# Kernel optimization log

Measured on AMD Instinct MI355X. Metric: run time of the kernel, lower is better.

The kernel has to match this reference:

```python
import jax, jax.numpy as jnp
import numpy as np

H = 56; W = 56; WS = 7; SHIFT = 3; HEADS = 4; C = 128; B = 64
N = WS * WS            # 49 tokens per window
NW = (H // WS) * (W // WS)  # 64 windows per image
HD = C // HEADS
EPS = 1e-5


def _rel_index():
    # matches get_relative_index: pairwise coord diffs in [-(WS-1), WS-1];
    # torch negative indexing wraps, so take mod (2*WS-1)
    coords = np.array([[i, j] for i in range(WS) for j in range(WS)])
    rel = coords[None, :, :] - coords[:, None, :]          # (N, N, 2)
    return (rel % (2 * WS - 1)).astype(np.int32)


def _attn_mask():
    # matches get_attn_mask for shifted windows
    img = np.zeros((H, W))
    sl = (slice(0, -WS), slice(-WS, -SHIFT), slice(-SHIFT, None))
    cnt = 0
    for hs in sl:
        for ws_ in sl:
            img[hs, ws_] = cnt
            cnt += 1
    m = img.reshape(H // WS, WS, W // WS, WS).transpose(0, 2, 1, 3).reshape(NW, N)
    am = m[:, None, :] - m[:, :, None]                     # (NW, N, N)
    return np.where(am != 0, -100.0, 0.0).astype(np.float32)

_REL_IDX = _rel_index()
_MASK = _attn_mask()


def _layernorm(x, g, b):
    mu = jnp.mean(x, axis=-1, keepdims=True)
    var = jnp.mean(jnp.square(x - mu), axis=-1, keepdims=True)
    return (x - mu) * jax.lax.rsqrt(var + EPS) * g + b


def setup_inputs() -> dict:
    key = jax.random.key(0)
    ks = jax.random.split(key, 16)
    s = 0.02
    return {
        "x": jax.random.normal(ks[0], (B, H * W, C), jnp.float32),
        "wq": jax.random.normal(ks[1], (C, C), jnp.float32) * s,
        "bq": jnp.zeros((C,), jnp.float32),
        "wk": jax.random.normal(ks[2], (C, C), jnp.float32) * s,
        "bk": jnp.zeros((C,), jnp.float32),
        "wv": jax.random.normal(ks[3], (C, C), jnp.float32) * s,
        "bv": jnp.zeros((C,), jnp.float32),
        "wo": jax.random.normal(ks[4], (C, C), jnp.float32) * s,
        "bo": jnp.zeros((C,), jnp.float32),
        "rel_table": jax.random.normal(ks[5], (2 * WS - 1, 2 * WS - 1, HEADS), jnp.float32) * s,
        "ln1_g": jnp.ones((C,), jnp.float32),
        "ln1_b": jnp.zeros((C,), jnp.float32),
        "ln2_g": jnp.ones((C,), jnp.float32),
        "ln2_b": jnp.zeros((C,), jnp.float32),
        "w1": jax.random.normal(ks[6], (C, 4 * C), jnp.float32) * s,
        "b1": jnp.zeros((4 * C,), jnp.float32),
        "w2": jax.random.normal(ks[7], (4 * C, C), jnp.float32) * s,
        "b2": jnp.zeros((C,), jnp.float32),
    }


def reference(x, wq, bq, wk, bk, wv, bv, wo, bo, rel_table,
              ln1_g, ln1_b, ln2_g, ln2_b, w1, b1, w2, b2):
    shortcut = x                                     # (B, H*W, C)
    h = _layernorm(x, ln1_g, ln1_b).reshape(B, H, W, C)
    h = jnp.roll(h, (-SHIFT, -SHIFT), axis=(1, 2))   # cyclic shift
    # window partition -> (B*NW, N, C)
    h = h.reshape(B, H // WS, WS, W // WS, WS, C).transpose(0, 1, 3, 2, 4, 5)
    h = h.reshape(B * NW, N, C)
    q = (h @ wq + bq).reshape(B * NW, N, HEADS, HD)
    k = (h @ wk + bk).reshape(B * NW, N, HEADS, HD)
    v = (h @ wv + bv).reshape(B * NW, N, HEADS, HD)
    attn = jnp.einsum('nqhd,nkhd->nhqk', q, k) / np.sqrt(HD).astype(np.float32)
    bias = rel_table[_REL_IDX[:, :, 0], _REL_IDX[:, :, 1]]  # (N, N, HEADS)
    attn = attn + jnp.transpose(bias, (2, 0, 1))[None]      # (1, H, N, N)
    # shifted-window additive mask
    attn = attn.reshape(B, NW, HEADS, N, N) + jnp.asarray(_MASK)[None, :, None]
    attn = jax.nn.softmax(attn.reshape(B * NW, HEADS, N, N), axis=-1)
    out = jnp.einsum('nhqk,nkhd->nqhd', attn, v).reshape(B * NW, N, C)
    out = out @ wo + bo
    # faithful to source bug: output taken directly from window-ordered tokens
    h = out.reshape(B, H * W, C)
    h = h + shortcut
    m = _layernorm(h, ln2_g, ln2_b)
    m = jax.nn.gelu(m @ w1 + b1, approximate=False) @ w2 + b2
    return h + m
```

## Files before the change

kernel.cpp:

```cpp
#include <hip/hip_runtime.h>

typedef __attribute__((ext_vector_type(8))) short short8;
typedef __attribute__((ext_vector_type(4))) float f32x4;
typedef unsigned short u16;
typedef unsigned int u32;

#define MFMA16(a, b, c) __builtin_amdgcn_mfma_f32_16x16x32_bf16((a), (b), (c), 0, 0, 0)
#define SCALE_Q 0.1767766952966369f

__device__ __forceinline__ u16 f2bf(float x) {
  u32 u = __float_as_uint(x);
  u32 r = u + 0x7FFF + ((u >> 16) & 1);
  return (u16)(r >> 16);
}

__device__ __forceinline__ void stage128(u16* lds, const u16* __restrict__ g, int stride, int tid) {
#pragma unroll
  for (int it = 0; it < 8; ++it) {
    int i = it * 256 + tid;
    int row = i >> 4, slot = i & 15;
    short8 v = *(const short8*)(g + row * stride + slot * 8);
    int byte_ = ((row << 8) + (slot << 4)) ^ ((row & 7) << 4);
    *(short8*)((char*)lds + byte_) = v;
  }
}

__device__ __forceinline__ short8 fld256(const u16* lds, int row, int kb) {
  int byte_ = ((row << 8) + kb) ^ ((row & 7) << 4);
  return *(const short8*)((const char*)lds + byte_);
}

__device__ __forceinline__ float gelu_f(float x) {
  float u = 0.7978845608f * (x + 0.044715f * x * x * x);
  float e = __expf(2.f * u);
  float t = 1.f - 2.f / (e + 1.f);
  return 0.5f * x * (1.f + t);
}

__global__ __launch_bounds__(256) void k0_weights(
    const float* __restrict__ wq, const float* __restrict__ wk, const float* __restrict__ wv,
    const float* __restrict__ wo, const float* __restrict__ w1, const float* __restrict__ w2,
    const float* __restrict__ bq, const float* __restrict__ bk, const float* __restrict__ bv,
    u16* __restrict__ wqkvt, u16* __restrict__ wot, u16* __restrict__ w1t, u16* __restrict__ w2t,
    float* __restrict__ bqkv) {
  int idx = blockIdx.x * 256 + threadIdx.x;
  if (idx < 49152) {
    int n = idx >> 7, k = idx & 127;
    float v;
    if (n < 128) v = wq[k * 128 + n] * SCALE_Q;
    else if (n < 256) v = wk[k * 128 + (n - 128)];
    else v = wv[k * 128 + (n - 256)];
    wqkvt[idx] = f2bf(v);
  } else if (idx < 65536) {
    int j = idx - 49152;
    int n = j >> 7, k = j & 127;
    wot[j] = f2bf(wo[k * 128 + n]);
  } else if (idx < 131072) {
    int j = idx - 65536;
    int n = j >> 7, k = j & 127;
    w1t[j] = f2bf(w1[k * 512 + n]);
  } else if (idx < 196608) {
    int j = idx - 131072;
    int n = j >> 9, k = j & 511;
    w2t[j] = f2bf(w2[k * 128 + n]);
  } else if (idx < 196992) {
    int n = idx - 196608;
    float v;
    if (n < 128) v = bq[n] * SCALE_Q;
    else if (n < 256) v = bk[n - 128];
    else v = bv[n - 256];
    bqkv[n] = v;
  }
}

__global__ __launch_bounds__(256) void k0_biasmask(const float* __restrict__ rel, float* __restrict__ bm) {
  int idx = blockIdx.x * 256 + threadIdx.x;
  int reg = idx & 3;
  int lane = (idx >> 2) & 63;
  int nt = (idx >> 8) & 3;
  int mt = (idx >> 10) & 3;
  int h = (idx >> 12) & 3;
  int wi = idx >> 14;
  int r = mt * 16 + ((lane >> 4) << 2) + reg;
  int c = nt * 16 + (lane & 15);
  float v = -1e30f;
  if (r < 49 && c < 49) {
    int qr = r / 7, qc = r % 7, kr = c / 7, kc = c % 7;
    int i0 = (kr - qr + 13) % 13, i1 = (kc - qc + 13) % 13;
    v = rel[(i0 * 13 + i1) * 4 + h];
    int gh = (wi >> 3) * 7 + qr, gw = (wi & 7) * 7 + qc;
    int kh = (wi >> 3) * 7 + kr, kw = (wi & 7) * 7 + kc;
    int rq = (gh < 49 ? 0 : (gh < 53 ? 1 : 2)) * 3 + (gw < 49 ? 0 : (gw < 53 ? 1 : 2));
    int rk = (kh < 49 ? 0 : (kh < 53 ? 1 : 2)) * 3 + (kw < 49 ? 0 : (kw < 53 ? 1 : 2));
    if (rq != rk) v -= 100.f;
  }
  bm[idx] = v;
}

__global__ __launch_bounds__(256) void k1_ln1(const float* __restrict__ x, const float* __restrict__ g,
                                              const float* __restrict__ b, u16* __restrict__ hwin) {
  int wid = threadIdx.x >> 6, lane = threadIdx.x & 63;
  int t = blockIdx.x * 4 + wid;
  float2 v = *(const float2*)(x + t * 128 + lane * 2);
  float s = v.x + v.y;
#pragma unroll
  for (int o = 1; o < 64; o <<= 1) s += __shfl_xor(s, o);
  float mu = s * 0.0078125f;
  float dx = v.x - mu, dy = v.y - mu;
  float q = dx * dx + dy * dy;
#pragma unroll
  for (int o = 1; o < 64; o <<= 1) q += __shfl_xor(q, o);
  float rstd = rsqrtf(q * 0.0078125f + 1e-5f);
  float y0 = dx * rstd * g[lane * 2] + b[lane * 2];
  float y1 = dy * rstd * g[lane * 2 + 1] + b[lane * 2 + 1];
  int bi = t / 3136, hw = t - bi * 3136;
  int oh = hw / 56, ow = hw - oh * 56;
  int gh = oh - 3; if (gh < 0) gh += 56;
  int gw = ow - 3; if (gw < 0) gw += 56;
  int win = bi * 64 + (gh / 7) * 8 + gw / 7;
  int n = (gh % 7) * 7 + (gw % 7);
  u32 packed = (u32)f2bf(y0) | ((u32)f2bf(y1) << 16);
  *(u32*)(hwin + (win * 49 + n) * 128 + lane * 2) = packed;
}

__global__ __launch_bounds__(256) void k2_qkv(const u16* __restrict__ hwin, const u16* __restrict__ wt,
                                              const float* __restrict__ bqkv, u16* __restrict__ qb,
                                              u16* __restrict__ kb, u16* __restrict__ vt) {
  __shared__ u16 lA[128 * 128];
  __shared__ u16 lB[128 * 128];
  int tid = threadIdx.x, mb = blockIdx.x, nb = blockIdx.y;
  stage128(lA, hwin + mb * 128 * 128, 128, tid);
  stage128(lB, wt + nb * 128 * 128, 128, tid);
  __syncthreads();
  int lane = tid & 63, w = tid >> 6;
  int wr = (w >> 1) * 64, wc = (w & 1) * 64;
  int g = lane >> 4, l15 = lane & 15;
  const f32x4 vz = {0.f, 0.f, 0.f, 0.f};
  f32x4 acc[4][4];
#pragma unroll
  for (int i = 0; i < 4; ++i)
#pragma unroll
    for (int j = 0; j < 4; ++j) acc[i][j] = vz;
#pragma unroll
  for (int kt = 0; kt < 4; ++kt) {
    short8 a[4], bfr[4];
#pragma unroll
    for (int mt = 0; mt < 4; ++mt) a[mt] = fld256(lA, wr + mt * 16 + l15, kt * 64 + g * 16);
#pragma unroll
    for (int nt = 0; nt < 4; ++nt) bfr[nt] = fld256(lB, wc + nt * 16 + l15, kt * 64 + g * 16);
#pragma unroll
    for (int mt = 0; mt < 4; ++mt)
#pragma unroll
      for (int nt = 0; nt < 4; ++nt) acc[mt][nt] = MFMA16(a[mt], bfr[nt], acc[mt][nt]);
  }
#pragma unroll
  for (int mt = 0; mt < 4; ++mt)
#pragma unroll
    for (int nt = 0; nt < 4; ++nt) {
      int ng = nb * 128 + wc + nt * 16 + l15;
      float bias = bqkv[ng];
#pragma unroll
      for (int reg = 0; reg < 4; ++reg) {
        int token = mb * 128 + wr + mt * 16 + g * 4 + reg;
        u16 hv = f2bf(acc[mt][nt][reg] + bias);
        if (nb == 0) qb[token * 128 + ng] = hv;
        else if (nb == 1) kb[token * 128 + ng - 128] = hv;
        else {
          int c = ng - 256;
          int win = token / 49, nn = token - win * 49;
          vt[win * 8192 + c * 64 + nn] = hv;
        }
      }
    }
}

__global__ __launch_bounds__(256) void k3_attn(const u16* __restrict__ qb, const u16* __restrict__ kb,
                                               const u16* __restrict__ vt, const float* __restrict__ bm,
                                               u16* __restrict__ ao) {
  __shared__ u16 pl[4 * 4096];
  int win = blockIdx.x;
  int lane = threadIdx.x & 63, head = threadIdx.x >> 6;
  int g = lane >> 4, l15 = lane & 15;
  u16* myp = pl + head * 4096;
  short8 aq[4], bk_[4];
#pragma unroll
  for (int mt = 0; mt < 4; ++mt)
    aq[mt] = *(const short8*)(qb + (win * 49 + mt * 16 + l15) * 128 + head * 32 + g * 8);
#pragma unroll
  for (int nt = 0; nt < 4; ++nt)
    bk_[nt] = *(const short8*)(kb + (win * 49 + nt * 16 + l15) * 128 + head * 32 + g * 8);
  const f32x4* bmv = (const f32x4*)bm + ((win & 63) * 4 + head) * 1024;
  f32x4 s[4][4];
#pragma unroll
  for (int mt = 0; mt < 4; ++mt)
#pragma unroll
    for (int nt = 0; nt < 4; ++nt) s[mt][nt] = bmv[(mt * 4 + nt) * 64 + lane];
#pragma unroll
  for (int mt = 0; mt < 4; ++mt)
#pragma unroll
    for (int nt = 0; nt < 4; ++nt) s[mt][nt] = MFMA16(aq[mt], bk_[nt], s[mt][nt]);
#pragma unroll
  for (int mt = 0; mt < 4; ++mt)
#pragma unroll
    for (int reg = 0; reg < 4; ++reg) {
      float m = fmaxf(fmaxf(s[mt][0][reg], s[mt][1][reg]), fmaxf(s[mt][2][reg], s[mt][3][reg]));
#pragma unroll
      for (int o = 1; o < 16; o <<= 1) m = fmaxf(m, __shfl_xor(m, o));
      float p0 = __expf(s[mt][0][reg] - m);
      float p1 = __expf(s[mt][1][reg] - m);
      float p2 = __expf(s[mt][2][reg] - m);
      float p3 = __expf(s[mt][3][reg] - m);
      float sum = p0 + p1 + p2 + p3;
#pragma unroll
      for (int o = 1; o < 16; o <<= 1) sum += __shfl_xor(sum, o);
      float rinv = 1.f / sum;
      s[mt][0][reg] = p0 * rinv; s[mt][1][reg] = p1 * rinv;
      s[mt][2][reg] = p2 * rinv; s[mt][3][reg] = p3 * rinv;
    }
#pragma unroll
  for (int mt = 0; mt < 4; ++mt)
#pragma unroll
    for (int nt = 0; nt < 4; ++nt)
#pragma unroll
      for (int reg = 0; reg < 4; ++reg) {
        int r = mt * 16 + g * 4 + reg, c = nt * 16 + l15;
        int byte_ = ((r << 7) + (c << 1)) ^ ((r & 7) << 4);
        *(u16*)((char*)myp + byte_) = f2bf(s[mt][nt][reg]);
      }
  __syncthreads();
  short8 vb[2][2];
#pragma unroll
  for (int kk = 0; kk < 2; ++kk)
#pragma unroll
    for (int n2 = 0; n2 < 2; ++n2)
      vb[kk][n2] = *(const short8*)(vt + win * 8192 + (head * 32 + n2 * 16 + l15) * 64 + kk * 32 + g * 8);
  const f32x4 vz = {0.f, 0.f, 0.f, 0.f};
  f32x4 o[4][2];
#pragma unroll
  for (int mt = 0; mt < 4; ++mt) { o[mt][0] = vz; o[mt][1] = vz; }
#pragma unroll
  for (int mt = 0; mt < 4; ++mt)
#pragma unroll
    for (int kk = 0; kk < 2; ++kk) {
      int r = mt * 16 + l15;
      int byte_ = ((r << 7) + kk * 64 + g * 16) ^ ((r & 7) << 4);
      short8 pa = *(const short8*)((const char*)myp + byte_);
#pragma unroll
      for (int n2 = 0; n2 < 2; ++n2) o[mt][n2] = MFMA16(pa, vb[kk][n2], o[mt][n2]);
    }
#pragma unroll
  for (int mt = 0; mt < 4; ++mt)
#pragma unroll
    for (int n2 = 0; n2 < 2; ++n2)
#pragma unroll
      for (int reg = 0; reg < 4; ++reg) {
        int r = mt * 16 + g * 4 + reg;
        if (r < 49) ao[(win * 49 + r) * 128 + head * 32 + n2 * 16 + l15] = f2bf(o[mt][n2][reg]);
      }
}

__global__ __launch_bounds__(256) void k4_proj(const u16* __restrict__ ao, const u16* __restrict__ wot,
                                               const float* __restrict__ bo, const float* __restrict__ x,
                                               const float* __restrict__ g2, const float* __restrict__ b2,
                                               float* __restrict__ dout, u16* __restrict__ ln2) {
  __shared__ u16 lA[128 * 128];
  __shared__ u16 lB[128 * 128];
  int tid = threadIdx.x, mb = blockIdx.x;
  stage128(lA, ao + mb * 128 * 128, 128, tid);
  stage128(lB, wot, 128, tid);
  __syncthreads();
  int lane = tid & 63, w = tid >> 6, g = lane >> 4, l15 = lane & 15;
  const f32x4 vz = {0.f, 0.f, 0.f, 0.f};
  f32x4 acc[2][8];
#pragma unroll
  for (int i = 0; i < 2; ++i)
#pragma unroll
    for (int j = 0; j < 8; ++j) acc[i][j] = vz;
#pragma unroll
  for (int kt = 0; kt < 4; ++kt) {
    short8 a[2], bfr[8];
#pragma unroll
    for (int mt = 0; mt < 2; ++mt) a[mt] = fld256(lA, w * 32 + mt * 16 + l15, kt * 64 + g * 16);
#pragma unroll
    for (int nt = 0; nt < 8; ++nt) bfr[nt] = fld256(lB, nt * 16 + l15, kt * 64 + g * 16);
#pragma unroll
    for (int mt = 0; mt < 2; ++mt)
#pragma unroll
      for (int nt = 0; nt < 8; ++nt) acc[mt][nt] = MFMA16(a[mt], bfr[nt], acc[mt][nt]);
  }
#pragma unroll
  for (int mt = 0; mt < 2; ++mt)
#pragma unroll
    for (int reg = 0; reg < 4; ++reg) {
      int token = mb * 128 + w * 32 + mt * 16 + g * 4 + reg;
      float hv[8];
      float s1 = 0.f, s2 = 0.f;
#pragma unroll
      for (int nt = 0; nt < 8; ++nt) {
        int c = nt * 16 + l15;
        float v = acc[mt][nt][reg] + bo[c] + x[token * 128 + c];
        dout[token * 128 + c] = v;
        hv[nt] = v; s1 += v; s2 += v * v;
      }
#pragma unroll
      for (int o = 1; o < 16; o <<= 1) { s1 += __shfl_xor(s1, o); s2 += __shfl_xor(s2, o); }
      float mu = s1 * 0.0078125f;
      float rstd = rsqrtf(fmaxf(s2 * 0.0078125f - mu * mu, 0.f) + 1e-5f);
#pragma unroll
      for (int nt = 0; nt < 8; ++nt) {
        int c = nt * 16 + l15;
        ln2[token * 128 + c] = f2bf((hv[nt] - mu) * rstd * g2[c] + b2[c]);
      }
    }
}

__global__ __launch_bounds__(256) void k5_mlp1(const u16* __restrict__ ln2, const u16* __restrict__ w1t,
                                               const float* __restrict__ b1, u16* __restrict__ g1) {
  __shared__ u16 lA[128 * 128];
  __shared__ u16 lB[128 * 128];
  int tid = threadIdx.x, mb = blockIdx.x, nb = blockIdx.y;
  stage128(lA, ln2 + mb * 128 * 128, 128, tid);
  stage128(lB, w1t + nb * 128 * 128, 128, tid);
  __syncthreads();
  int lane = tid & 63, w = tid >> 6;
  int wr = (w >> 1) * 64, wc = (w & 1) * 64;
  int g = lane >> 4, l15 = lane & 15;
  const f32x4 vz = {0.f, 0.f, 0.f, 0.f};
  f32x4 acc[4][4];
#pragma unroll
  for (int i = 0; i < 4; ++i)
#pragma unroll
    for (int j = 0; j < 4; ++j) acc[i][j] = vz;
#pragma unroll
  for (int kt = 0; kt < 4; ++kt) {
    short8 a[4], bfr[4];
#pragma unroll
    for (int mt = 0; mt < 4; ++mt) a[mt] = fld256(lA, wr + mt * 16 + l15, kt * 64 + g * 16);
#pragma unroll
    for (int nt = 0; nt < 4; ++nt) bfr[nt] = fld256(lB, wc + nt * 16 + l15, kt * 64 + g * 16);
#pragma unroll
    for (int mt = 0; mt < 4; ++mt)
#pragma unroll
      for (int nt = 0; nt < 4; ++nt) acc[mt][nt] = MFMA16(a[mt], bfr[nt], acc[mt][nt]);
  }
#pragma unroll
  for (int mt = 0; mt < 4; ++mt)
#pragma unroll
    for (int nt = 0; nt < 4; ++nt) {
      int ng = nb * 128 + wc + nt * 16 + l15;
      float bias = b1[ng];
#pragma unroll
      for (int reg = 0; reg < 4; ++reg) {
        int token = mb * 128 + wr + mt * 16 + g * 4 + reg;
        g1[token * 512 + ng] = f2bf(gelu_f(acc[mt][nt][reg] + bias));
      }
    }
}

__global__ __launch_bounds__(256) void k6_mlp2(const u16* __restrict__ g1, const u16* __restrict__ w2t,
                                               const float* __restrict__ b2, float* __restrict__ dout) {
  __shared__ u16 lA[128 * 128];
  __shared__ u16 lB[128 * 128];
  int tid = threadIdx.x, mb = blockIdx.x;
  int lane = tid & 63, w = tid >> 6;
  int wr = (w >> 1) * 64, wc = (w & 1) * 64;
  int g = lane >> 4, l15 = lane & 15;
  const f32x4 vz = {0.f, 0.f, 0.f, 0.f};
  f32x4 acc[4][4];
#pragma unroll
  for (int i = 0; i < 4; ++i)
#pragma unroll
    for (int j = 0; j < 4; ++j) acc[i][j] = vz;
  for (int kc = 0; kc < 4; ++kc) {
    if (kc) __syncthreads();
    stage128(lA, g1 + mb * (128 * 512) + kc * 128, 512, tid);
    stage128(lB, w2t + kc * 128, 512, tid);
    __syncthreads();
#pragma unroll
    for (int kt = 0; kt < 4; ++kt) {
      short8 a[4], bfr[4];
#pragma unroll
      for (int mt = 0; mt < 4; ++mt) a[mt] = fld256(lA, wr + mt * 16 + l15, kt * 64 + g * 16);
#pragma unroll
      for (int nt = 0; nt < 4; ++nt) bfr[nt] = fld256(lB, wc + nt * 16 + l15, kt * 64 + g * 16);
#pragma unroll
      for (int mt = 0; mt < 4; ++mt)
#pragma unroll
        for (int nt = 0; nt < 4; ++nt) acc[mt][nt] = MFMA16(a[mt], bfr[nt], acc[mt][nt]);
    }
  }
#pragma unroll
  for (int mt = 0; mt < 4; ++mt)
#pragma unroll
    for (int nt = 0; nt < 4; ++nt) {
      int ng = wc + nt * 16 + l15;
      float bias = b2[ng];
#pragma unroll
      for (int reg = 0; reg < 4; ++reg) {
        int token = mb * 128 + wr + mt * 16 + g * 4 + reg;
        int i = token * 128 + ng;
        dout[i] = acc[mt][nt][reg] + bias + dout[i];
      }
    }
}

extern "C" void kernel_launch(void* const* d_in, const int* in_sizes, int n_in,
                              void* d_out, int out_size, void* d_ws, size_t ws_size,
                              hipStream_t stream) {
  const float* x    = (const float*)d_in[0];
  const float* wq   = (const float*)d_in[1];
  const float* bq   = (const float*)d_in[2];
  const float* wk   = (const float*)d_in[3];
  const float* bk   = (const float*)d_in[4];
  const float* wv   = (const float*)d_in[5];
  const float* bv   = (const float*)d_in[6];
  const float* wo   = (const float*)d_in[7];
  const float* bo   = (const float*)d_in[8];
  const float* rel  = (const float*)d_in[9];
  const float* ln1g = (const float*)d_in[10];
  const float* ln1b = (const float*)d_in[11];
  const float* ln2g = (const float*)d_in[12];
  const float* ln2b = (const float*)d_in[13];
  const float* w1   = (const float*)d_in[14];
  const float* b1   = (const float*)d_in[15];
  const float* w2   = (const float*)d_in[16];
  const float* b2   = (const float*)d_in[17];
  float* out = (float*)d_out;
  char* ws = (char*)d_ws;

  const size_t TOK = 200704;
  float* bmask = (float*)(ws);
  u16* wqkvt = (u16*)(ws + (size_t)(4 << 20));
  u16* wot   = (u16*)(ws + (size_t)(4 << 20) + 196608);
  u16* w1t   = (u16*)(ws + (size_t)(4 << 20) + 229376);
  u16* w2t   = (u16*)(ws + (size_t)(4 << 20) + 360448);
  float* bqkv = (float*)(ws + (size_t)(4 << 20) + 491520);
  const size_t SB = TOK * 128 * 2;
  u16* hwin = (u16*)(ws + (size_t)(8 << 20));
  u16* qb   = (u16*)(ws + (size_t)(8 << 20) + SB);
  u16* kb   = (u16*)(ws + (size_t)(8 << 20) + 2 * SB);
  u16* vt   = (u16*)(ws + (size_t)(8 << 20) + 3 * SB);
  u16* attn = hwin;
  u16* ln2  = qb;
  u16* g1b  = kb;

  k0_weights<<<770, 256, 0, stream>>>(wq, wk, wv, wo, w1, w2, bq, bk, bv,
                                      wqkvt, wot, w1t, w2t, bqkv);
  k0_biasmask<<<4096, 256, 0, stream>>>(rel, bmask);
  k1_ln1<<<50176, 256, 0, stream>>>(x, ln1g, ln1b, hwin);
  k2_qkv<<<dim3(1568, 3), dim3(256), 0, stream>>>(hwin, wqkvt, bqkv, qb, kb, vt);
  k3_attn<<<4096, 256, 0, stream>>>(qb, kb, vt, bmask, attn);
  k4_proj<<<1568, 256, 0, stream>>>(attn, wot, bo, x, ln2g, ln2b, out, ln2);
  k5_mlp1<<<dim3(1568, 4), dim3(256), 0, stream>>>(ln2, w1t, b1, g1b);
  k6_mlp2<<<1568, 256, 0, stream>>>(g1b, w2t, b2, out);
}
```

Baseline: 839.0 us.

## Drop LDS staging in GEMM kernels; keep A rows in registers and loop over N

All four GEMM kernels (qkv, proj, mlp1, mlp2) stop staging tiles through shared memory. Each wave now owns 64 token rows and loads its A fragments straight from global memory into registers. It then loops over all output column blocks, reading weight fragments directly from global or L2. This removes the LDS writes, barriers and redundant re-reads of the activation tile across the grid.y column blocks. In exchange it uses more registers, may lower occupancy, and relies on the cache for the weight reads that shared memory used to serve.

```diff
diff --git a/kernel.cpp b/kernel.cpp
--- a/kernel.cpp
+++ b/kernel.cpp
@@ -12,22 +12,6 @@
   u32 u = __float_as_uint(x);
   u32 r = u + 0x7FFF + ((u >> 16) & 1);
   return (u16)(r >> 16);
-}
-
-__device__ __forceinline__ void stage128(u16* lds, const u16* __restrict__ g, int stride, int tid) {
-#pragma unroll
-  for (int it = 0; it < 8; ++it) {
-    int i = it * 256 + tid;
-    int row = i >> 4, slot = i & 15;
-    short8 v = *(const short8*)(g + row * stride + slot * 8);
-    int byte_ = ((row << 8) + (slot << 4)) ^ ((row & 7) << 4);
-    *(short8*)((char*)lds + byte_) = v;
-  }
-}
-
-__device__ __forceinline__ short8 fld256(const u16* lds, int row, int kb) {
-  int byte_ = ((row << 8) + kb) ^ ((row & 7) << 4);
-  return *(const short8*)((const char*)lds + byte_);
 }
 
 __device__ __forceinline__ float gelu_f(float x) {
@@ -126,52 +110,53 @@
 __global__ __launch_bounds__(256) void k2_qkv(const u16* __restrict__ hwin, const u16* __restrict__ wt,
                                               const float* __restrict__ bqkv, u16* __restrict__ qb,
                                               u16* __restrict__ kb, u16* __restrict__ vt) {
-  __shared__ u16 lA[128 * 128];
-  __shared__ u16 lB[128 * 128];
-  int tid = threadIdx.x, mb = blockIdx.x, nb = blockIdx.y;
-  stage128(lA, hwin + mb * 128 * 128, 128, tid);
-  stage128(lB, wt + nb * 128 * 128, 128, tid);
-  __syncthreads();
-  int lane = tid & 63, w = tid >> 6;
-  int wr = (w >> 1) * 64, wc = (w & 1) * 64;
+  int tid = threadIdx.x, lane = tid & 63, w = tid >> 6;
   int g = lane >> 4, l15 = lane & 15;
+  int row0 = blockIdx.x * 256 + w * 64;
+  short8 a[4][4];
+#pragma unroll
+  for (int mt = 0; mt < 4; ++mt)
+#pragma unroll
+    for (int kt = 0; kt < 4; ++kt)
+      a[mt][kt] = *(const short8*)(hwin + (size_t)(row0 + mt * 16 + l15) * 128 + kt * 32 + g * 8);
   const f32x4 vz = {0.f, 0.f, 0.f, 0.f};
-  f32x4 acc[4][4];
-#pragma unroll
-  for (int i = 0; i < 4; ++i)
-#pragma unroll
-    for (int j = 0; j < 4; ++j) acc[i][j] = vz;
-#pragma unroll
-  for (int kt = 0; kt < 4; ++kt) {
-    short8 a[4], bfr[4];
-#pragma unroll
-    for (int mt = 0; mt < 4; ++mt) a[mt] = fld256(lA, wr + mt * 16 + l15, kt * 64 + g * 16);
-#pragma unroll
-    for (int nt = 0; nt < 4; ++nt) bfr[nt] = fld256(lB, wc + nt * 16 + l15, kt * 64 + g * 16);
+  for (int nb = 0; nb < 6; ++nb) {
+    f32x4 acc[4][4];
+#pragma unroll
+    for (int i = 0; i < 4; ++i)
+#pragma unroll
+      for (int j = 0; j < 4; ++j) acc[i][j] = vz;
+#pragma unroll
+    for (int kt = 0; kt < 4; ++kt) {
+      short8 bfr[4];
+#pragma unroll
+      for (int nt = 0; nt < 4; ++nt)
+        bfr[nt] = *(const short8*)(wt + (size_t)(nb * 64 + nt * 16 + l15) * 128 + kt * 32 + g * 8);
+#pragma unroll
+      for (int mt = 0; mt < 4; ++mt)
+#pragma unroll
+        for (int nt = 0; nt < 4; ++nt) acc[mt][nt] = MFMA16(a[mt][kt], bfr[nt], acc[mt][nt]);
+    }
 #pragma unroll
     for (int mt = 0; mt < 4; ++mt)
 #pragma unroll
-      for (int nt = 0; nt < 4; ++nt) acc[mt][nt] = MFMA16(a[mt], bfr[nt], acc[mt][nt]);
-  }
-#pragma unroll
-  for (int mt = 0; mt < 4; ++mt)
-#pragma unroll
-    for (int nt = 0; nt < 4; ++nt) {
-      int ng = nb * 128 + wc + nt * 16 + l15;
-      float bias = bqkv[ng];
-#pragma unroll
-      for (int reg = 0; reg < 4; ++reg) {
-        int token = mb * 128 + wr + mt * 16 + g * 4 + reg;
-        u16 hv = f2bf(acc[mt][nt][reg] + bias);
-        if (nb == 0) qb[token * 128 + ng] = hv;
-        else if (nb == 1) kb[token * 128 + ng - 128] = hv;
-        else {
-          int c = ng - 256;
-          int win = token / 49, nn = token - win * 49;
-          vt[win * 8192 + c * 64 + nn] = hv;
+      for (int nt = 0; nt < 4; ++nt) {
+        int ng = nb * 64 + nt * 16 + l15;
+        float bias = bqkv[ng];
+#pragma unroll
+        for (int reg = 0; reg < 4; ++reg) {
+          int token = row0 + mt * 16 + g * 4 + reg;
+          u16 hv = f2bf(acc[mt][nt][reg] + bias);
+          if (nb < 2) qb[(size_t)token * 128 + ng] = hv;
+          else if (nb < 4) kb[(size_t)token * 128 + ng - 128] = hv;
+          else {
+            int c = ng - 256;
+            int win = token / 49, nn = token - win * 49;
+            vt[(size_t)win * 8192 + c * 64 + nn] = hv;
+          }
         }
       }
-    }
+  }
 }
 
 __global__ __launch_bounds__(256) void k3_attn(const u16* __restrict__ qb, const u16* __restrict__ kb,
@@ -185,10 +170,10 @@
   short8 aq[4], bk_[4];
 #pragma unroll
   for (int mt = 0; mt < 4; ++mt)
-    aq[mt] = *(const short8*)(qb + (win * 49 + mt * 16 + l15) * 128 + head * 32 + g * 8);
+    aq[mt] = *(const short8*)(qb + (size_t)(win * 49 + mt * 16 + l15) * 128 + head * 32 + g * 8);
 #pragma unroll
   for (int nt = 0; nt < 4; ++nt)
-    bk_[nt] = *(const short8*)(kb + (win * 49 + nt * 16 + l15) * 128 + head * 32 + g * 8);
+    bk_[nt] = *(const short8*)(kb + (size_t)(win * 49 + nt * 16 + l15) * 128 + head * 32 + g * 8);
   const f32x4* bmv = (const f32x4*)bm + ((win & 63) * 4 + head) * 1024;
   f32x4 s[4][4];
 #pragma unroll
@@ -233,7 +218,7 @@
   for (int kk = 0; kk < 2; ++kk)
 #pragma unroll
     for (int n2 = 0; n2 < 2; ++n2)
-      vb[kk][n2] = *(const short8*)(vt + win * 8192 + (head * 32 + n2 * 16 + l15) * 64 + kk * 32 + g * 8);
+      vb[kk][n2] = *(const short8*)(vt + (size_t)win * 8192 + (head * 32 + n2 * 16 + l15) * 64 + kk * 32 + g * 8);
   const f32x4 vz = {0.f, 0.f, 0.f, 0.f};
   f32x4 o[4][2];
 #pragma unroll
@@ -255,7 +240,7 @@
 #pragma unroll
       for (int reg = 0; reg < 4; ++reg) {
         int r = mt * 16 + g * 4 + reg;
-        if (r < 49) ao[(win * 49 + r) * 128 + head * 32 + n2 * 16 + l15] = f2bf(o[mt][n2][reg]);
+        if (r < 49) ao[(size_t)(win * 49 + r) * 128 + head * 32 + n2 * 16 + l15] = f2bf(o[mt][n2][reg]);
       }
 }
 
@@ -263,43 +248,44 @@
                                                const float* __restrict__ bo, const float* __restrict__ x,
                                                const float* __restrict__ g2, const float* __restrict__ b2,
                                                float* __restrict__ dout, u16* __restrict__ ln2) {
-  __shared__ u16 lA[128 * 128];
-  __shared__ u16 lB[128 * 128];
-  int tid = threadIdx.x, mb = blockIdx.x;
-  stage128(lA, ao + mb * 128 * 128, 128, tid);
-  stage128(lB, wot, 128, tid);
-  __syncthreads();
-  int lane = tid & 63, w = tid >> 6, g = lane >> 4, l15 = lane & 15;
+  int tid = threadIdx.x, lane = tid & 63, w = tid >> 6;
+  int g = lane >> 4, l15 = lane & 15;
+  int row0 = blockIdx.x * 256 + w * 64;
+  short8 a[4][4];
+#pragma unroll
+  for (int mt = 0; mt < 4; ++mt)
+#pragma unroll
+    for (int kt = 0; kt < 4; ++kt)
+      a[mt][kt] = *(const short8*)(ao + (size_t)(row0 + mt * 16 + l15) * 128 + kt * 32 + g * 8);
   const f32x4 vz = {0.f, 0.f, 0.f, 0.f};
-  f32x4 acc[2][8];
-#pragma unroll
-  for (int i = 0; i < 2; ++i)
+  f32x4 acc[4][8];
+#pragma unroll
+  for (int i = 0; i < 4; ++i)
 #pragma unroll
     for (int j = 0; j < 8; ++j) acc[i][j] = vz;
 #pragma unroll
   for (int kt = 0; kt < 4; ++kt) {
-    short8 a[2], bfr[8];
-#pragma unroll
-    for (int mt = 0; mt < 2; ++mt) a[mt] = fld256(lA, w * 32 + mt * 16 + l15, kt * 64 + g * 16);
-#pragma unroll
-    for (int nt = 0; nt < 8; ++nt) bfr[nt] = fld256(lB, nt * 16 + l15, kt * 64 + g * 16);
-#pragma unroll
-    for (int mt = 0; mt < 2; ++mt)
-#pragma unroll
-      for (int nt = 0; nt < 8; ++nt) acc[mt][nt] = MFMA16(a[mt], bfr[nt], acc[mt][nt]);
-  }
-#pragma unroll
-  for (int mt = 0; mt < 2; ++mt)
+    short8 bfr[8];
+#pragma unroll
+    for (int nt = 0; nt < 8; ++nt)
+      bfr[nt] = *(const short8*)(wot + (size_t)(nt * 16 + l15) * 128 + kt * 32 + g * 8);
+#pragma unroll
+    for (int mt = 0; mt < 4; ++mt)
+#pragma unroll
+      for (int nt = 0; nt < 8; ++nt) acc[mt][nt] = MFMA16(a[mt][kt], bfr[nt], acc[mt][nt]);
+  }
+#pragma unroll
+  for (int mt = 0; mt < 4; ++mt)
 #pragma unroll
     for (int reg = 0; reg < 4; ++reg) {
-      int token = mb * 128 + w * 32 + mt * 16 + g * 4 + reg;
+      int token = row0 + mt * 16 + g * 4 + reg;
       float hv[8];
       float s1 = 0.f, s2 = 0.f;
 #pragma unroll
       for (int nt = 0; nt < 8; ++nt) {
         int c = nt * 16 + l15;
-        float v = acc[mt][nt][reg] + bo[c] + x[token * 128 + c];
-        dout[token * 128 + c] = v;
+        float v = acc[mt][nt][reg] + bo[c] + x[(size_t)token * 128 + c];
+        dout[(size_t)token * 128 + c] = v;
         hv[nt] = v; s1 += v; s2 += v * v;
       }
 #pragma unroll
@@ -309,96 +295,91 @@
 #pragma unroll
       for (int nt = 0; nt < 8; ++nt) {
         int c = nt * 16 + l15;
-        ln2[token * 128 + c] = f2bf((hv[nt] - mu) * rstd * g2[c] + b2[c]);
+        ln2[(size_t)token * 128 + c] = f2bf((hv[nt] - mu) * rstd * g2[c] + b2[c]);
       }
     }
 }
 
 __global__ __launch_bounds__(256) void k5_mlp1(const u16* __restrict__ ln2, const u16* __restrict__ w1t,
                                                const float* __restrict__ b1, u16* __restrict__ g1) {
-  __shared__ u16 lA[128 * 128];
-  __shared__ u16 lB[128 * 128];
-  int tid = threadIdx.x, mb = blockIdx.x, nb = blockIdx.y;
-  stage128(lA, ln2 + mb * 128 * 128, 128, tid);
-  stage128(lB, w1t + nb * 128 * 128, 128, tid);
-  __syncthreads();
-  int lane = tid & 63, w = tid >> 6;
-  int wr = (w >> 1) * 64, wc = (w & 1) * 64;
+  int tid = threadIdx.x, lane = tid & 63, w = tid >> 6;
   int g = lane >> 4, l15 = lane & 15;
+  int row0 = blockIdx.x * 256 + w * 64;
+  short8 a[4][4];
+#pragma unroll
+  for (int mt = 0; mt < 4; ++mt)
+#pragma unroll
+    for (int kt = 0; kt < 4; ++kt)
+      a[mt][kt] = *(const short8*)(ln2 + (size_t)(row0 + mt * 16 + l15) * 128 + kt * 32 + g * 8);
   const f32x4 vz = {0.f, 0.f, 0.f, 0.f};
-  f32x4 acc[4][4];
-#pragma unroll
-  for (int i = 0; i < 4; ++i)
-#pragma unroll
-    for (int j = 0; j < 4; ++j) acc[i][j] = vz;
-#pragma unroll
-  for (int kt = 0; kt < 4; ++kt) {
-    short8 a[4], bfr[4];
-#pragma unroll
-    for (int mt = 0; mt < 4; ++mt) a[mt] = fld256(lA, wr + mt * 16 + l15, kt * 64 + g * 16);
-#pragma unroll
-    for (int nt = 0; nt < 4; ++nt) bfr[nt] = fld256(lB, wc + nt * 16 + l15, kt * 64 + g * 16);
+  for (int nb = 0; nb < 8; ++nb) {
+    f32x4 acc[4][4];
+#pragma unroll
+    for (int i = 0; i < 4; ++i)
+#pragma unroll
+      for (int j = 0; j < 4; ++j) acc[i][j] = vz;
+#pragma unroll
+    for (int kt = 0; kt < 4; ++kt) {
+      short8 bfr[4];
+#pragma unroll
+      for (int nt = 0; nt < 4; ++nt)
+        bfr[nt] = *(const short8*)(w1t + (size_t)(nb * 64 + nt * 16 + l15) * 128 + kt * 32 + g * 8);
+#pragma unroll
+      for (int mt = 0; mt < 4; ++mt)
+#pragma unroll
+        for (int nt = 0; nt < 4; ++nt) acc[mt][nt] = MFMA16(a[mt][kt], bfr[nt], acc[mt][nt]);
+    }
 #pragma unroll
     for (int mt = 0; mt < 4; ++mt)
 #pragma unroll
-      for (int nt = 0; nt < 4; ++nt) acc[mt][nt] = MFMA16(a[mt], bfr[nt], acc[mt][nt]);
-  }
-#pragma unroll
-  for (int mt = 0; mt < 4; ++mt)
-#pragma unroll
-    for (int nt = 0; nt < 4; ++nt) {
-      int ng = nb * 128 + wc + nt * 16 + l15;
-      float bias = b1[ng];
-#pragma unroll
-      for (int reg = 0; reg < 4; ++reg) {
-        int token = mb * 128 + wr + mt * 16 + g * 4 + reg;
-        g1[token * 512 + ng] = f2bf(gelu_f(acc[mt][nt][reg] + bias));
-      }
-    }
+      for (int nt = 0; nt < 4; ++nt) {
+        int ng = nb * 64 + nt * 16 + l15;
+        float bias = b1[ng];
+#pragma unroll
+        for (int reg = 0; reg < 4; ++reg) {
+          int token = row0 + mt * 16 + g * 4 + reg;
+          g1[(size_t)token * 512 + ng] = f2bf(gelu_f(acc[mt][nt][reg] + bias));
+        }
+      }
+  }
 }
 
 __global__ __launch_bounds__(256) void k6_mlp2(const u16* __restrict__ g1, const u16* __restrict__ w2t,
                                                const float* __restrict__ b2, float* __restrict__ dout) {
-  __shared__ u16 lA[128 * 128];
-  __shared__ u16 lB[128 * 128];
-  int tid = threadIdx.x, mb = blockIdx.x;
-  int lane = tid & 63, w = tid >> 6;
-  int wr = (w >> 1) * 64, wc = (w & 1) * 64;
+  int tid = threadIdx.x, lane = tid & 63, w = tid >> 6;
   int g = lane >> 4, l15 = lane & 15;
+  int row0 = blockIdx.x * 256 + w * 64;
   const f32x4 vz = {0.f, 0.f, 0.f, 0.f};
-  f32x4 acc[4][4];
+  f32x4 acc[4][8];
 #pragma unroll
   for (int i = 0; i < 4; ++i)
 #pragma unroll
-    for (int j = 0; j < 4; ++j) acc[i][j] = vz;
-  for (int kc = 0; kc < 4; ++kc) {
-    if (kc) __syncthreads();
-    stage128(lA, g1 + mb * (128 * 512) + kc * 128, 512, tid);
-    stage128(lB, w2t + kc * 128, 512, tid);
-    __syncthreads();
-#pragma unroll
-    for (int kt = 0; kt < 4; ++kt) {
-      short8 a[4], bfr[4];
-#pragma unroll
-      for (int mt = 0; mt < 4; ++mt) a[mt] = fld256(lA, wr + mt * 16 + l15, kt * 64 + g * 16);
-#pragma unroll
-      for (int nt = 0; nt < 4; ++nt) bfr[nt] = fld256(lB, wc + nt * 16 + l15, kt * 64 + g * 16);
-#pragma unroll
-      for (int mt = 0; mt < 4; ++mt)
-#pragma unroll
-        for (int nt = 0; nt < 4; ++nt) acc[mt][nt] = MFMA16(a[mt], bfr[nt], acc[mt][nt]);
-    }
-  }
-#pragma unroll
-  for (int mt = 0; mt < 4; ++mt)
-#pragma unroll
-    for (int nt = 0; nt < 4; ++nt) {
-      int ng = wc + nt * 16 + l15;
-      float bias = b2[ng];
+    for (int j = 0; j < 8; ++j) acc[i][j] = vz;
+#pragma unroll
+  for (int kt = 0; kt < 16; ++kt) {
+    short8 a[4];
+#pragma unroll
+    for (int mt = 0; mt < 4; ++mt)
+      a[mt] = *(const short8*)(g1 + (size_t)(row0 + mt * 16 + l15) * 512 + kt * 32 + g * 8);
+    short8 bfr[8];
+#pragma unroll
+    for (int nt = 0; nt < 8; ++nt)
+      bfr[nt] = *(const short8*)(w2t + (size_t)(nt * 16 + l15) * 512 + kt * 32 + g * 8);
+#pragma unroll
+    for (int mt = 0; mt < 4; ++mt)
+#pragma unroll
+      for (int nt = 0; nt < 8; ++nt) acc[mt][nt] = MFMA16(a[mt], bfr[nt], acc[mt][nt]);
+  }
+#pragma unroll
+  for (int mt = 0; mt < 4; ++mt)
+#pragma unroll
+    for (int nt = 0; nt < 8; ++nt) {
+      int c = nt * 16 + l15;
+      float bias = b2[c];
 #pragma unroll
       for (int reg = 0; reg < 4; ++reg) {
-        int token = mb * 128 + wr + mt * 16 + g * 4 + reg;
-        int i = token * 128 + ng;
+        int token = row0 + mt * 16 + g * 4 + reg;
+        size_t i = (size_t)token * 128 + c;
         dout[i] = acc[mt][nt][reg] + bias + dout[i];
       }
     }
@@ -448,9 +429,9 @@
                                       wqkvt, wot, w1t, w2t, bqkv);
   k0_biasmask<<<4096, 256, 0, stream>>>(rel, bmask);
   k1_ln1<<<50176, 256, 0, stream>>>(x, ln1g, ln1b, hwin);
-  k2_qkv<<<dim3(1568, 3), dim3(256), 0, stream>>>(hwin, wqkvt, bqkv, qb, kb, vt);
+  k2_qkv<<<784, 256, 0, stream>>>(hwin, wqkvt, bqkv, qb, kb, vt);
   k3_attn<<<4096, 256, 0, stream>>>(qb, kb, vt, bmask, attn);
-  k4_proj<<<1568, 256, 0, stream>>>(attn, wot, bo, x, ln2g, ln2b, out, ln2);
-  k5_mlp1<<<dim3(1568, 4), dim3(256), 0, stream>>>(ln2, w1t, b1, g1b);
-  k6_mlp2<<<1568, 256, 0, stream>>>(g1b, w2t, b2, out);
-}
+  k4_proj<<<784, 256, 0, stream>>>(attn, wot, bo, x, ln2g, ln2b, out, ln2);
+  k5_mlp1<<<784, 256, 0, stream>>>(ln2, w1t, b1, g1b);
+  k6_mlp2<<<784, 256, 0, stream>>>(g1b, w2t, b2, out);
+}
```

New measurement: 892.3 us. +6.3%, slower.
